# Kernel optimization log

Hardware: AMD Instinct MI355X
Metric: run time of the kernel (lower is better)

## Reference

```python
import jax, jax.numpy as jnp
import numpy as np

EPS = 1e-6

def _ln(x, g, b):
    mu = jnp.mean(x, axis=-1, keepdims=True)
    var = jnp.mean(jnp.square(x - mu), axis=-1, keepdims=True)
    return (x - mu) * jax.lax.rsqrt(var + EPS) * g + b

def setup_inputs() -> dict:
    key = jax.random.key(0)
    ks = jax.random.split(key, 8)
    B, S, D, H, HD, F = 4, 1024, 1024, 16, 64, 4096
    s = 0.02
    return {
        "hidden_state": jax.random.normal(ks[0], (B, S, D), jnp.float32),
        "mask": jnp.ones((B, S), jnp.int32),
        "Wq": jax.random.normal(ks[1], (H, D, HD), jnp.float32) * s,
        "bq": jnp.zeros((H, HD), jnp.float32),
        "Wk": jax.random.normal(ks[2], (H, D, HD), jnp.float32) * s,
        "bk": jnp.zeros((H, HD), jnp.float32),
        "Wv": jax.random.normal(ks[3], (H, D, HD), jnp.float32) * s,
        "bv": jnp.zeros((H, HD), jnp.float32),
        "Wo": jax.random.normal(ks[4], (D, D), jnp.float32) * s,
        "bo": jnp.zeros((D,), jnp.float32),
        "ln1_g": jnp.ones((D,), jnp.float32),
        "ln1_b": jnp.zeros((D,), jnp.float32),
        "ln2_g": jnp.ones((D,), jnp.float32),
        "ln2_b": jnp.zeros((D,), jnp.float32),
        "W1": jax.random.normal(ks[5], (D, F), jnp.float32) * s,
        "b1": jnp.zeros((F,), jnp.float32),
        "W2": jax.random.normal(ks[6], (F, D), jnp.float32) * s,
        "b2": jnp.zeros((D,), jnp.float32),
    }

def reference(hidden_state, mask, Wq, bq, Wk, bk, Wv, bv, Wo, bo,
              ln1_g, ln1_b, ln2_g, ln2_b, W1, b1, W2, b2):
    # Pre-norm
    x1 = _ln(hidden_state, ln1_g, ln1_b)  # [B,S,D]
    # Per-head projections stacked over head axis h
    q = jnp.einsum('bsd,hdk->bhsk', x1, Wq) + bq[:, None, :]
    k = jnp.einsum('bsd,hdk->bhsk', x1, Wk) + bk[:, None, :]
    v = jnp.einsum('bsd,hdk->bhsk', x1, Wv) + bv[:, None, :]
    head_dim = q.shape[-1]
    scores = jnp.einsum('bhqk,bhsk->bhqs', q, k) / jnp.sqrt(jnp.float32(head_dim))
    scores = jnp.where(mask[:, None, None, :] == 0, jnp.float32(-1e9), scores)
    w = jax.nn.softmax(scores, axis=-1)
    attn = jnp.einsum('bhqs,bhsk->bhqk', w, v)  # [B,H,S,HD]
    B, H, S, HD = attn.shape
    attn = attn.transpose(0, 2, 1, 3).reshape(B, S, H * HD)  # concat heads
    attn = attn @ Wo + bo
    h = attn + hidden_state
    x2 = _ln(h, ln2_g, ln2_b)
    ff = jax.nn.gelu(x2 @ W1 + b1, approximate=False) @ W2 + b2
    return ff + h
```

## Files before the change

kernel.cpp:

```cpp
#include <hip/hip_runtime.h>

typedef __bf16 bf16;
typedef __bf16 bf16x4 __attribute__((ext_vector_type(4)));
typedef __bf16 bf16x8 __attribute__((ext_vector_type(8)));
typedef float  f32x4  __attribute__((ext_vector_type(4)));

#define F32X4_ZERO ((f32x4){0.f, 0.f, 0.f, 0.f})

__device__ __forceinline__ f32x4 mfma16(bf16x8 a, bf16x8 b, f32x4 c) {
  return __builtin_amdgcn_mfma_f32_16x16x32_bf16(a, b, c, 0, 0, 0);
}

__device__ __forceinline__ void gld16(const void* g, void* l) {
  __builtin_amdgcn_global_load_lds((const __attribute__((address_space(1))) void*)g,
                                   (__attribute__((address_space(3))) void*)l, 16, 0, 0);
}

__device__ __forceinline__ float gelu_f(float u) {
  return 0.5f * u * (1.0f + erff(u * 0.70710678118654752f));
}

__device__ __forceinline__ bf16x8 frag_ld(const bf16* base, int row, int c16) {
  return *(const bf16x8*)((const char*)base + row * 128 + (((c16) ^ (row & 7)) << 4));
}

__device__ __forceinline__ bf16x8 frag_ld32(const bf16* base, int row, int c16) {
  return *(const bf16x8*)((const char*)base + row * 64 + ((c16 ^ ((row >> 1) & 3)) << 4));
}
#define WAITB(N) asm volatile("s_waitcnt vmcnt(" #N ")\ns_barrier" ::: "memory")

__global__ void transpose2(const float* __restrict__ src, size_t sBatch, int sStride,
                           bf16* __restrict__ dst, size_t dBatch, int dStride) {
  __shared__ bf16 t[32][33];
  src += (size_t)blockIdx.z * sBatch;
  dst += (size_t)blockIdx.z * dBatch;
  int c0 = blockIdx.x * 32, r0 = blockIdx.y * 32;
#pragma unroll
  for (int i = 0; i < 4; i++) {
    int r = threadIdx.y + i * 8;
    t[r][threadIdx.x] = (bf16)src[(size_t)(r0 + r) * sStride + c0 + threadIdx.x];
  }
  __syncthreads();
#pragma unroll
  for (int i = 0; i < 4; i++) {
    int c = threadIdx.y + i * 8;
    dst[(size_t)(c0 + c) * dStride + r0 + threadIdx.x] = t[threadIdx.x][c];
  }
}

__global__ __launch_bounds__(256) void ln_rows(const float* __restrict__ in,
                                               const float* __restrict__ gam,
                                               const float* __restrict__ bet,
                                               bf16* __restrict__ out) {
  int row = blockIdx.x, tid = threadIdx.x;
  f32x4 x = *(const f32x4*)(in + (size_t)row * 1024 + tid * 4);
  float s = 0.f, q = 0.f;
#pragma unroll
  for (int j = 0; j < 4; j++) { s += x[j]; q += x[j] * x[j]; }
#pragma unroll
  for (int o = 1; o < 64; o <<= 1) {
    s += __shfl_xor(s, o, 64);
    q += __shfl_xor(q, o, 64);
  }
  __shared__ float red[8];
  if ((tid & 63) == 0) { red[(tid >> 6) * 2] = s; red[(tid >> 6) * 2 + 1] = q; }
  __syncthreads();
  s = red[0] + red[2] + red[4] + red[6];
  q = red[1] + red[3] + red[5] + red[7];
  float mean = s * (1.f / 1024.f);
  float var  = q * (1.f / 1024.f) - mean * mean;
  float inv  = rsqrtf(var + 1e-6f);
  bf16x4 o;
#pragma unroll
  for (int j = 0; j < 4; j++) {
    int c = tid * 4 + j;
    o[j] = (bf16)((x[j] - mean) * inv * gam[c] + bet[c]);
  }
  *(bf16x4*)(out + (size_t)row * 1024 + tid * 4) = o;
}

enum { EPI_WO = 0, EPI_GELU = 1, EPI_ACC0 = 2, EPI_ACC = 3, EPI_FINAL = 4 };

template <int EPI, int K, int NTL>
__global__ __launch_bounds__(256) void pipe128(
    const bf16* __restrict__ A, const bf16* __restrict__ BT, const float* __restrict__ bias,
    int N,
    const float* __restrict__ resid, float* __restrict__ facc,
    bf16* __restrict__ outb, float* __restrict__ outf) {
  int tid = threadIdx.x, lane = tid & 63, wv = tid >> 6;
  int bid = blockIdx.x + (blockIdx.y << 3);
  int xcd = bid & 7, idx = bid >> 3;
  int m0 = (xcd * 4 + (idx >> NTL)) * 128;
  int n0 = (idx & ((1 << NTL) - 1)) * 128;
  int wrow = (wv >> 1) * 64, wcol = (wv & 1) * 64;
  __shared__ __align__(16) bf16 lds[3][8192];
  f32x4 acc[4][4];
#pragma unroll
  for (int a = 0; a < 4; a++)
#pragma unroll
    for (int n = 0; n < 4; n++) acc[a][n] = F32X4_ZERO;

  constexpr int nk = K / 32;
  int rin = lane >> 2;
  int sbc = ((lane & 3) ^ ((lane >> 3) & 3)) * 16;
  auto stage = [&](int slot, int k0) {
#pragma unroll
    for (int j = 0; j < 4; j++) {
      int c = wv * 4 + j;
      if (c < 8)
        gld16((const char*)A + ((size_t)(m0 + c * 16 + rin) * K + k0) * 2 + sbc,
              (char*)lds[slot] + c * 1024);
      else
        gld16((const char*)BT + ((size_t)(n0 + (c - 8) * 16 + rin) * K + k0) * 2 + sbc,
              (char*)lds[slot] + c * 1024);
    }
  };

  stage(0, 0); stage(1, 32);
#pragma unroll 1
  for (int t = 0; t < nk; t++) {
    if (t < nk - 1) WAITB(4);
    else            WAITB(0);
    if (t + 2 < nk) stage((t + 2) % 3, (t + 2) * 32);
    const bf16* As = lds[t % 3];
    const bf16* Bs = lds[t % 3] + 4096;
    int c16 = lane >> 4;
    bf16x8 af[4], bfr[4];
#pragma unroll
    for (int mf = 0; mf < 4; mf++)
      af[mf] = frag_ld32(As, wrow + mf * 16 + (lane & 15), c16);
#pragma unroll
    for (int nf = 0; nf < 4; nf++)
      bfr[nf] = frag_ld32(Bs, wcol + nf * 16 + (lane & 15), c16);
#pragma unroll
    for (int mf = 0; mf < 4; mf++)
#pragma unroll
      for (int nf = 0; nf < 4; nf++)
        acc[mf][nf] = mfma16(af[mf], bfr[nf], acc[mf][nf]);
  }
#pragma unroll
  for (int mf = 0; mf < 4; mf++)
#pragma unroll
    for (int nf = 0; nf < 4; nf++)
#pragma unroll
      for (int i = 0; i < 4; i++) {
        int row = m0 + wrow + mf * 16 + ((lane >> 4) << 2) + i;
        int col = n0 + wcol + nf * 16 + (lane & 15);
        size_t idx2 = (size_t)row * N + col;
        float v = acc[mf][nf][i];
        if constexpr (EPI == EPI_WO) {
          outf[idx2] = v + bias[col] + resid[idx2];
        } else if constexpr (EPI == EPI_GELU) {
          outb[idx2] = (bf16)gelu_f(v + bias[col]);
        } else if constexpr (EPI == EPI_ACC0) {
          facc[idx2] = v;
        } else if constexpr (EPI == EPI_ACC) {
          facc[idx2] += v;
        } else {
          outf[idx2] = facc[idx2] + v + bias[col] + resid[idx2];
        }
      }
}

__global__ __launch_bounds__(256) void qkv_pipe(
    const bf16* __restrict__ x1,
    const bf16* __restrict__ WqT, const bf16* __restrict__ WkT, const bf16* __restrict__ WvT,
    const float* __restrict__ bq, const float* __restrict__ bk, const float* __restrict__ bv,
    bf16* __restrict__ qo, bf16* __restrict__ ko, bf16* __restrict__ vto) {
  int tid = threadIdx.x, lane = tid & 63, wv = tid >> 6;
  int z = blockIdx.z;
  const bf16* BT; const float* bias;
  if (z == 0)      { BT = WqT; bias = bq; }
  else if (z == 1) { BT = WkT; bias = bk; }
  else             { BT = WvT; bias = bv; }
  int bid = blockIdx.x + (blockIdx.y << 3);
  int xcd = bid & 7, idx = bid >> 3;
  int m0 = (xcd * 4 + (idx >> 3)) * 128, n0 = (idx & 7) * 128;
  int wrow = (wv >> 1) * 64, wcol = (wv & 1) * 64;
  __shared__ __align__(16) bf16 lds[3][8192];
  f32x4 acc[4][4];
#pragma unroll
  for (int a = 0; a < 4; a++)
#pragma unroll
    for (int n = 0; n < 4; n++) acc[a][n] = F32X4_ZERO;

  constexpr int K = 1024, nk = K / 32;
  int rin = lane >> 2;
  int sbc = ((lane & 3) ^ ((lane >> 3) & 3)) * 16;
  auto stage = [&](int slot, int k0) {
#pragma unroll
    for (int j = 0; j < 4; j++) {
      int c = wv * 4 + j;
      if (c < 8)
        gld16((const char*)x1 + ((size_t)(m0 + c * 16 + rin) * K + k0) * 2 + sbc,
              (char*)lds[slot] + c * 1024);
      else
        gld16((const char*)BT + ((size_t)(n0 + (c - 8) * 16 + rin) * K + k0) * 2 + sbc,
              (char*)lds[slot] + c * 1024);
    }
  };

  stage(0, 0); stage(1, 32);
#pragma unroll 1
  for (int t = 0; t < nk; t++) {
    if (t < nk - 1) WAITB(4);
    else            WAITB(0);
    if (t + 2 < nk) stage((t + 2) % 3, (t + 2) * 32);
    const bf16* As = lds[t % 3];
    const bf16* Bs = lds[t % 3] + 4096;
    int c16 = lane >> 4;
    bf16x8 af[4], bfr[4];
#pragma unroll
    for (int mf = 0; mf < 4; mf++)
      af[mf] = frag_ld32(As, wrow + mf * 16 + (lane & 15), c16);
#pragma unroll
    for (int nf = 0; nf < 4; nf++)
      bfr[nf] = frag_ld32(Bs, wcol + nf * 16 + (lane & 15), c16);
#pragma unroll
    for (int mf = 0; mf < 4; mf++)
#pragma unroll
      for (int nf = 0; nf < 4; nf++)
        acc[mf][nf] = mfma16(af[mf], bfr[nf], acc[mf][nf]);
  }
#pragma unroll
  for (int mf = 0; mf < 4; mf++)
#pragma unroll
    for (int nf = 0; nf < 4; nf++)
#pragma unroll
      for (int i = 0; i < 4; i++) {
        int row  = m0 + wrow + mf * 16 + ((lane >> 4) << 2) + i;
        int ncol = n0 + wcol + nf * 16 + (lane & 15);
        int bb = row >> 10, s = row & 1023, head = ncol >> 6, d = ncol & 63;
        size_t bh = (size_t)bb * 16 + head;
        float v = acc[mf][nf][i] + bias[ncol];
        if (z == 0)      qo[(bh * 1024 + s) * 64 + d] = (bf16)(v * 0.125f);
        else if (z == 1) ko[(bh * 1024 + s) * 64 + d] = (bf16)v;
        else             vto[(bh * 64 + d) * 1024 + s] = (bf16)v;
      }
}

__global__ __launch_bounds__(512) void attn_flash(
    const bf16* __restrict__ qb, const bf16* __restrict__ kb, const bf16* __restrict__ vtb,
    const int* __restrict__ mask, bf16* __restrict__ attnC) {
  int tid = threadIdx.x, lane = tid & 63, wv = tid >> 6;
  int wgid = blockIdx.x;
  int nid  = (wgid & 7) * 64 + (wgid >> 3);
  int qblk = nid & 7, h = (nid >> 3) & 15, b = nid >> 7;
  int qrow0 = qblk * 128 + wv * 16;

  __shared__ float smask[1024];
  __shared__ __align__(16) bf16 kt[2][64 * 64];
  __shared__ __align__(16) bf16 vt[2][64 * 64];
  __shared__ __align__(16) bf16 pb[8][16][72];
  for (int i = tid; i < 1024; i += 512) smask[i] = mask[b * 1024 + i] ? 0.f : -1e9f;

  size_t bh = (size_t)b * 16 + h;
  const bf16* qp = qb + (bh * 1024 + qrow0) * 64;
  bf16x8 qa[2];
#pragma unroll
  for (int kc = 0; kc < 2; kc++)
    qa[kc] = *(const bf16x8*)(qp + (lane & 15) * 64 + kc * 32 + (lane >> 4) * 8);

  const bf16* kp = kb + bh * 1024 * 64;
  const bf16* vp = vtb + bh * 64 * 1024;
  bf16* myp = &pb[wv][0][0];

  bf16x8 vone;
#pragma unroll
  for (int j = 0; j < 8; j++) vone[j] = (bf16)1.0f;

  f32x4 ssum = F32X4_ZERO;
  f32x4 oacc[4];
#pragma unroll
  for (int i = 0; i < 4; i++) oacc[i] = F32X4_ZERO;

  int srl = lane >> 3;
  int sbc = ((lane & 7) ^ srl) * 16;
  auto stage = [&](int buf, int t2) {
    int key0n = t2 * 64;
#pragma unroll
    for (int j = 0; j < 2; j++) {
      int c = wv * 2 + j;
      if (c < 8) {
        int row = c * 8 + srl;
        gld16((const char*)kp + ((size_t)(key0n + row) * 64) * 2 + sbc,
              (char*)kt[buf] + c * 1024);
      } else {
        int row = (c - 8) * 8 + srl;
        gld16((const char*)vp + ((size_t)row * 1024 + key0n) * 2 + sbc,
              (char*)vt[buf] + (c - 8) * 1024);
      }
    }
  };

  stage(0, 0);
  __syncthreads();

  for (int t = 0; t < 16; t++) {
    int cur = t & 1;
    if (t < 15) stage(cur ^ 1, t + 1);
    const bf16* kcur = kt[cur];
    const bf16* vcur = vt[cur];
    int key0 = t * 64;
    f32x4 st[4];
    __builtin_amdgcn_s_setprio(1);
#pragma unroll
    for (int nt = 0; nt < 4; nt++) {
      st[nt] = F32X4_ZERO;
#pragma unroll
      for (int kc = 0; kc < 2; kc++) {
        bf16x8 kf = frag_ld(kcur, nt * 16 + (lane & 15), kc * 4 + (lane >> 4));
        st[nt] = mfma16(qa[kc], kf, st[nt]);
      }
    }
    __builtin_amdgcn_s_setprio(0);
#pragma unroll
    for (int nt = 0; nt < 4; nt++) {
      float ms = smask[key0 + nt * 16 + (lane & 15)] - 8.0f;
#pragma unroll
      for (int i = 0; i < 4; i++) st[nt][i] = __expf(st[nt][i] + ms);
    }
#pragma unroll
    for (int nt = 0; nt < 4; nt++)
#pragma unroll
      for (int i = 0; i < 4; i++)
        myp[((lane >> 4) * 4 + i) * 72 + nt * 16 + (lane & 15)] = (bf16)st[nt][i];
    __builtin_amdgcn_s_setprio(1);
#pragma unroll
    for (int kc = 0; kc < 2; kc++) {
      bf16x8 pa = *(const bf16x8*)(myp + (lane & 15) * 72 + kc * 32 + (lane >> 4) * 8);
      ssum = mfma16(pa, vone, ssum);
#pragma unroll
      for (int dn = 0; dn < 4; dn++) {
        bf16x8 vf = frag_ld(vcur, dn * 16 + (lane & 15), kc * 4 + (lane >> 4));
        oacc[dn] = mfma16(pa, vf, oacc[dn]);
      }
    }
    __builtin_amdgcn_s_setprio(0);
    __syncthreads();
  }
#pragma unroll
  for (int i = 0; i < 4; i++) {
    float inv = 1.0f / ssum[i];
    int row = qrow0 + ((lane >> 4) << 2) + i;
#pragma unroll
    for (int dn = 0; dn < 4; dn++)
      attnC[(size_t)(b * 1024 + row) * 1024 + h * 64 + dn * 16 + (lane & 15)] =
          (bf16)(oacc[dn][i] * inv);
  }
}

template <int EPI, int K>
__global__ __launch_bounds__(256) void gemm_bt(
    const bf16* __restrict__ A, const bf16* __restrict__ BT, const float* __restrict__ bias,
    int N,
    const float* __restrict__ resid, float* __restrict__ facc,
    bf16* __restrict__ outb, float* __restrict__ outf) {
  int tid = threadIdx.x, lane = tid & 63, wv = tid >> 6;
  int m0 = blockIdx.y * 128, n0 = blockIdx.x * 128;
  int wrow = (wv >> 1) * 64, wcol = (wv & 1) * 64;
  __shared__ __align__(16) bf16 lA[2][128 * 64];
  __shared__ __align__(16) bf16 lB[2][128 * 64];
  f32x4 acc[4][4];
#pragma unroll
  for (int a = 0; a < 4; a++)
#pragma unroll
    for (int n = 0; n < 4; n++) acc[a][n] = F32X4_ZERO;

  int cbs = ((lane & 7) ^ (lane >> 3)) * 16;
  auto stage = [&](int buf, int k0) {
#pragma unroll
    for (int s = 0; s < 4; s++) {
      int c = s * 4 + wv;
      int row = c * 8 + (lane >> 3);
      gld16((const char*)A  + ((size_t)(m0 + row) * K + k0) * 2 + cbs,
            (char*)lA[buf] + c * 1024);
      gld16((const char*)BT + ((size_t)(n0 + row) * K + k0) * 2 + cbs,
            (char*)lB[buf] + c * 1024);
    }
  };

  constexpr int nk = K >> 6;
  stage(0, 0);
  __syncthreads();
#pragma unroll 1
  for (int t = 0; t < nk; t++) {
    int cur = t & 1;
    if (t + 1 < nk) stage(cur ^ 1, (t + 1) * 64);
#pragma unroll
    for (int kc = 0; kc < 2; kc++) {
      int c16 = kc * 4 + (lane >> 4);
      bf16x8 af[4], bfr[4];
#pragma unroll
      for (int mf = 0; mf < 4; mf++)
        af[mf] = frag_ld(lA[cur], wrow + mf * 16 + (lane & 15), c16);
#pragma unroll
      for (int nf = 0; nf < 4; nf++)
        bfr[nf] = frag_ld(lB[cur], wcol + nf * 16 + (lane & 15), c16);
#pragma unroll
      for (int mf = 0; mf < 4; mf++)
#pragma unroll
        for (int nf = 0; nf < 4; nf++)
          acc[mf][nf] = mfma16(af[mf], bfr[nf], acc[mf][nf]);
    }
    __syncthreads();
  }
#pragma unroll
  for (int mf = 0; mf < 4; mf++)
#pragma unroll
    for (int nf = 0; nf < 4; nf++)
#pragma unroll
      for (int i = 0; i < 4; i++) {
        int row = m0 + wrow + mf * 16 + ((lane >> 4) << 2) + i;
        int col = n0 + wcol + nf * 16 + (lane & 15);
        size_t idx2 = (size_t)row * N + col;
        float v = acc[mf][nf][i];
        if constexpr (EPI == EPI_WO) {
          outf[idx2] = v + bias[col] + resid[idx2];
        } else if constexpr (EPI == EPI_GELU) {
          outb[idx2] = (bf16)gelu_f(v + bias[col]);
        } else if constexpr (EPI == EPI_ACC0) {
          facc[idx2] = v;
        } else if constexpr (EPI == EPI_ACC) {
          facc[idx2] += v;
        } else {
          outf[idx2] = facc[idx2] + v + bias[col] + resid[idx2];
        }
      }
}

extern "C" void kernel_launch(void* const* d_in, const int* in_sizes, int n_in,
                              void* d_out, int out_size, void* d_ws, size_t ws_size,
                              hipStream_t stream) {
  const float* hidden = (const float*)d_in[0];
  const int*   mask   = (const int*)d_in[1];
  const float* Wq = (const float*)d_in[2];
  const float* bq = (const float*)d_in[3];
  const float* Wk = (const float*)d_in[4];
  const float* bk = (const float*)d_in[5];
  const float* Wv = (const float*)d_in[6];
  const float* bv = (const float*)d_in[7];
  const float* Wo = (const float*)d_in[8];
  const float* bo = (const float*)d_in[9];
  const float* ln1g = (const float*)d_in[10];
  const float* ln1b = (const float*)d_in[11];
  const float* ln2g = (const float*)d_in[12];
  const float* ln2b = (const float*)d_in[13];
  const float* W1 = (const float*)d_in[14];
  const float* b1 = (const float*)d_in[15];
  const float* W2 = (const float*)d_in[16];
  const float* b2 = (const float*)d_in[17];
  float* out = (float*)d_out;

  char* ws = (char*)d_ws;
  const size_t MB = 1ull << 20;
  dim3 tb(32, 8);
  const size_t HB = 64 * 1024;

  if (ws_size >= 96 * MB) {
    bf16* x1    = (bf16*)(ws + 0 * MB);
    bf16* attnC = x1;
    bf16* x2    = x1;
    bf16* qbuf  = (bf16*)(ws + 8 * MB);
    bf16* W1T   = qbuf;
    bf16* kbuf  = (bf16*)(ws + 16 * MB);
    bf16* W2T   = kbuf;
    bf16* vtbuf = (bf16*)(ws + 24 * MB);
    float* hbuf = (float*)(ws + 32 * MB);
    bf16* WqT   = (bf16*)(ws + 48 * MB);
    bf16* WkT   = (bf16*)(ws + 50 * MB);
    bf16* WvT   = (bf16*)(ws + 52 * MB);
    bf16* WoT   = (bf16*)(ws + 54 * MB);
    bf16* gbuf  = (bf16*)(ws + 56 * MB);

    transpose2<<<dim3(2, 32, 16), tb, 0, stream>>>(Wq, HB, 64, WqT, HB, 1024);
    transpose2<<<dim3(2, 32, 16), tb, 0, stream>>>(Wk, HB, 64, WkT, HB, 1024);
    transpose2<<<dim3(2, 32, 16), tb, 0, stream>>>(Wv, HB, 64, WvT, HB, 1024);
    transpose2<<<dim3(32, 32, 1), tb, 0, stream>>>(Wo, 0, 1024, WoT, 0, 1024);
    ln_rows<<<4096, 256, 0, stream>>>(hidden, ln1g, ln1b, x1);
    qkv_pipe<<<dim3(8, 32, 3), 256, 0, stream>>>(x1, WqT, WkT, WvT, bq, bk, bv,
                                                 qbuf, kbuf, vtbuf);
    attn_flash<<<512, 512, 0, stream>>>(qbuf, kbuf, vtbuf, mask, attnC);
    pipe128<EPI_WO, 1024, 3><<<dim3(8, 32), 256, 0, stream>>>(attnC, WoT, bo, 1024,
                                                              hidden, nullptr, nullptr, hbuf);
    ln_rows<<<4096, 256, 0, stream>>>(hbuf, ln2g, ln2b, x2);
    transpose2<<<dim3(128, 32, 1), tb, 0, stream>>>(W1, 0, 4096, W1T, 0, 1024);
    transpose2<<<dim3(32, 128, 1), tb, 0, stream>>>(W2, 0, 1024, W2T, 0, 4096);
    pipe128<EPI_GELU, 1024, 5><<<dim3(8, 128), 256, 0, stream>>>(x2, W1T, b1, 4096,
                                                                 nullptr, nullptr, gbuf, nullptr);
    pipe128<EPI_WO, 4096, 3><<<dim3(8, 32), 256, 0, stream>>>(gbuf, W2T, b2, 1024,
                                                              hbuf, nullptr, nullptr, out);
  } else {
    bf16* x1     = (bf16*)(ws + 0 * MB);
    bf16* attnC  = x1;
    bf16* x2     = x1;
    bf16* qbuf   = (bf16*)(ws + 8 * MB);
    bf16* W1Tc   = (bf16*)(ws + 8 * MB);
    bf16* W2Tc   = (bf16*)(ws + 10 * MB);
    bf16* gchunk = (bf16*)(ws + 12 * MB);
    bf16* kbuf   = (bf16*)(ws + 16 * MB);
    bf16* vtbuf  = (bf16*)(ws + 24 * MB);
    float* hbuf  = (float*)(ws + 16 * MB);
    bf16* WqT    = (bf16*)(ws + 32 * MB);
    bf16* WkT    = (bf16*)(ws + 34 * MB);
    bf16* WvT    = (bf16*)(ws + 36 * MB);
    bf16* WoT    = (bf16*)(ws + 38 * MB);
    float* outacc = (float*)(ws + 40 * MB);

    transpose2<<<dim3(2, 32, 16), tb, 0, stream>>>(Wq, HB, 64, WqT, HB, 1024);
    transpose2<<<dim3(2, 32, 16), tb, 0, stream>>>(Wk, HB, 64, WkT, HB, 1024);
    transpose2<<<dim3(2, 32, 16), tb, 0, stream>>>(Wv, HB, 64, WvT, HB, 1024);
    transpose2<<<dim3(32, 32, 1), tb, 0, stream>>>(Wo, 0, 1024, WoT, 0, 1024);
    ln_rows<<<4096, 256, 0, stream>>>(hidden, ln1g, ln1b, x1);
    qkv_pipe<<<dim3(8, 32, 3), 256, 0, stream>>>(x1, WqT, WkT, WvT, bq, bk, bv,
                                                 qbuf, kbuf, vtbuf);
    attn_flash<<<512, 512, 0, stream>>>(qbuf, kbuf, vtbuf, mask, attnC);
    pipe128<EPI_WO, 1024, 3><<<dim3(8, 32), 256, 0, stream>>>(attnC, WoT, bo, 1024,
                                                              hidden, nullptr, nullptr, hbuf);
    ln_rows<<<4096, 256, 0, stream>>>(hbuf, ln2g, ln2b, x2);

    for (int c = 0; c < 8; c++) {
      transpose2<<<dim3(16, 32, 1), tb, 0, stream>>>(W1 + c * 512, 0, 4096,
                                                     W1Tc, 0, 1024);
      transpose2<<<dim3(32, 16, 1), tb, 0, stream>>>(W2 + (size_t)c * 512 * 1024, 0, 1024,
                                                     W2Tc, 0, 512);
      gemm_bt<EPI_GELU, 1024><<<dim3(4, 32), 256, 0, stream>>>(x2, W1Tc, b1 + c * 512, 512,
                                                               nullptr, nullptr, gchunk, nullptr);
      if (c == 0)
        gemm_bt<EPI_ACC0, 512><<<dim3(8, 32), 256, 0, stream>>>(gchunk, W2Tc, b2, 1024,
                                                                nullptr, outacc, nullptr, nullptr);
      else if (c < 7)
        gemm_bt<EPI_ACC, 512><<<dim3(8, 32), 256, 0, stream>>>(gchunk, W2Tc, b2, 1024,
                                                               nullptr, outacc, nullptr, nullptr);
      else
        gemm_bt<EPI_FINAL, 512><<<dim3(8, 32), 256, 0, stream>>>(gchunk, W2Tc, b2, 1024,
                                                                 hbuf, outacc, nullptr, out);
    }
  }

  (void)in_sizes; (void)n_in; (void)out_size;
}
```

Baseline: 231.4 us.

## Use 256x128 tile kernel with 8 waves for the W1 GELU GEMM

Adds a dedicated 512-thread GEMM kernel for the first FFN projection. Each block computes a 256x128 output tile with a triple-buffered LDS pipeline and remaps blocks onto XCDs by M/N groups. Larger tiles raise operand reuse and halve the block count, in exchange for more LDS per block and possibly lower occupancy.

```diff
diff --git a/kernel.cpp b/kernel.cpp
--- a/kernel.cpp
+++ b/kernel.cpp
@@ -80,6 +80,73 @@
 }
 
 enum { EPI_WO = 0, EPI_GELU = 1, EPI_ACC0 = 2, EPI_ACC = 3, EPI_FINAL = 4 };
+
+__global__ __launch_bounds__(512) void pipe256x128_gelu(
+    const bf16* __restrict__ A, const bf16* __restrict__ BT, const float* __restrict__ bias,
+    int N, bf16* __restrict__ outb) {
+  int tid = threadIdx.x, lane = tid & 63, wv = tid >> 6;
+  int bid = blockIdx.x;
+  int xcd = bid & 7, idx = bid >> 3;
+  int mg = xcd >> 1, ng = xcd & 1;
+  int m0 = (mg * 4 + (idx >> 4)) * 256;
+  int n0 = (ng * 16 + (idx & 15)) * 128;
+  int wrow = (wv >> 1) * 64, wcol = (wv & 1) * 64;
+  __shared__ __align__(16) bf16 lds[3][12288];
+  f32x4 acc[4][4];
+#pragma unroll
+  for (int a = 0; a < 4; a++)
+#pragma unroll
+    for (int n = 0; n < 4; n++) acc[a][n] = F32X4_ZERO;
+
+  constexpr int K = 1024, nk = K / 32;
+  int rin = lane >> 2;
+  int sbc = ((lane & 3) ^ ((lane >> 3) & 3)) * 16;
+  auto stage = [&](int slot, int k0) {
+#pragma unroll
+    for (int j = 0; j < 3; j++) {
+      int c = wv * 3 + j;
+      if (c < 16)
+        gld16((const char*)A + ((size_t)(m0 + c * 16 + rin) * K + k0) * 2 + sbc,
+              (char*)lds[slot] + c * 1024);
+      else
+        gld16((const char*)BT + ((size_t)(n0 + (c - 16) * 16 + rin) * K + k0) * 2 + sbc,
+              (char*)lds[slot] + c * 1024);
+    }
+  };
+
+  stage(0, 0); stage(1, 32);
+#pragma unroll 1
+  for (int t = 0; t < nk; t++) {
+    if (t < nk - 1) WAITB(3);
+    else            WAITB(0);
+    if (t + 2 < nk) stage((t + 2) % 3, (t + 2) * 32);
+    const bf16* As = lds[t % 3];
+    const bf16* Bs = lds[t % 3] + 8192;
+    int c16 = lane >> 4;
+    bf16x8 af[4], bfr[4];
+#pragma unroll
+    for (int mf = 0; mf < 4; mf++)
+      af[mf] = frag_ld32(As, wrow + mf * 16 + (lane & 15), c16);
+#pragma unroll
+    for (int nf = 0; nf < 4; nf++)
+      bfr[nf] = frag_ld32(Bs, wcol + nf * 16 + (lane & 15), c16);
+#pragma unroll
+    for (int mf = 0; mf < 4; mf++)
+#pragma unroll
+      for (int nf = 0; nf < 4; nf++)
+        acc[mf][nf] = mfma16(af[mf], bfr[nf], acc[mf][nf]);
+  }
+#pragma unroll
+  for (int mf = 0; mf < 4; mf++)
+#pragma unroll
+    for (int nf = 0; nf < 4; nf++)
+#pragma unroll
+      for (int i = 0; i < 4; i++) {
+        int row = m0 + wrow + mf * 16 + ((lane >> 4) << 2) + i;
+        int col = n0 + wcol + nf * 16 + (lane & 15);
+        outb[(size_t)row * N + col] = (bf16)gelu_f(acc[mf][nf][i] + bias[col]);
+      }
+}
 
 template <int EPI, int K, int NTL>
 __global__ __launch_bounds__(256) void pipe128(
@@ -486,8 +553,7 @@
     ln_rows<<<4096, 256, 0, stream>>>(hbuf, ln2g, ln2b, x2);
     transpose2<<<dim3(128, 32, 1), tb, 0, stream>>>(W1, 0, 4096, W1T, 0, 1024);
     transpose2<<<dim3(32, 128, 1), tb, 0, stream>>>(W2, 0, 1024, W2T, 0, 4096);
-    pipe128<EPI_GELU, 1024, 5><<<dim3(8, 128), 256, 0, stream>>>(x2, W1T, b1, 4096,
-                                                                 nullptr, nullptr, gbuf, nullptr);
+    pipe256x128_gelu<<<512, 512, 0, stream>>>(x2, W1T, b1, 4096, gbuf);
     pipe128<EPI_WO, 4096, 3><<<dim3(8, 32), 256, 0, stream>>>(gbuf, W2T, b2, 1024,
                                                               hbuf, nullptr, nullptr, out);
   } else {
```

After: 223.0 us (median of 2 runs). -3.6%, faster.
